# Kernel tuning notes

Measured on AMD Instinct MI355X. Metric: run time of the kernel, lower is better.

The kernel has to match this reference:

```python
import jax, jax.numpy as jnp
import numpy as np

NUM_TABLES = 26
NUM_ROWS = 50000
WIDTH = 128
BATCH = 4096
NNZ = 20
NUM_NUM = 13
MLP_SIZES = [512, 256, 128]


def setup_inputs() -> dict:
    key = jax.random.key(0)
    ks = jax.random.split(key, 16)
    numerical = jax.random.normal(ks[0], (BATCH, NUM_NUM), dtype=jnp.float32)
    cat = jax.random.randint(ks[1], (NUM_TABLES, BATCH, NNZ), 0, NUM_ROWS)
    tables = jax.random.normal(ks[2], (NUM_TABLES, NUM_ROWS, WIDTH), dtype=jnp.float32) * 0.01
    d_in = NUM_TABLES * WIDTH + NUM_NUM  # concat of pooled embeddings + numericals
    dims = [d_in] + MLP_SIZES + [1]
    inp = {"numerical": numerical, "cat": cat, "tables": tables}
    for i in range(len(dims) - 1):
        scale = 1.0 / np.sqrt(dims[i])
        inp[f"W{i+1}"] = jax.random.normal(ks[3 + i], (dims[i], dims[i + 1]), dtype=jnp.float32) * scale
        inp[f"b{i+1}"] = jnp.zeros((dims[i + 1],), dtype=jnp.float32)
    return inp


def reference(numerical, cat, tables, W1, b1, W2, b2, W3, b3, W4, b4):
    # Multi-table gather + reduce_sum: tables [T,R,W], cat [T,B,NNZ] -> pooled [T,B,W]
    pooled = jax.vmap(lambda T, idx: jnp.take(T, idx, axis=0).sum(axis=1))(tables, cat)
    # concat pooled tables (in input order) then numericals: [B, T*W + NUM_NUM]
    flat = pooled.transpose(1, 0, 2).reshape(pooled.shape[1], -1)
    x = jnp.concatenate([flat, numerical], axis=1)
    x = jax.nn.relu(x @ W1 + b1)
    x = jax.nn.relu(x @ W2 + b2)
    x = jax.nn.relu(x @ W3 + b3)
    return x @ W4 + b4  # [B, 1]
```

## Files before the change

kernel.cpp:

```cpp
#include <hip/hip_runtime.h>
#include <hip/hip_bf16.h>

#define T_NUM_TABLES 26
#define T_NUM_ROWS 50000
#define T_WIDTH 128
#define T_BATCH 4096
#define T_NNZ 20
#define T_NUM_NUM 13
#define T_DE (T_NUM_TABLES * T_WIDTH)

typedef __attribute__((ext_vector_type(4))) float f32x4;
typedef __attribute__((ext_vector_type(8))) short bf16x8;

#define PJ_POOL (512 * T_NUM_TABLES)
#define PJ_WT (PJ_POOL + 1664 + 128 + 32)
#define PJ_TOTAL (PJ_WT + T_BATCH)

__global__ void poolprep_v7(const float* __restrict__ tables,
                            const int* __restrict__ cat,
                            const float* __restrict__ W1, const float* __restrict__ W2,
                            const float* __restrict__ W3, const float* __restrict__ b1,
                            const float* __restrict__ b4, const float* __restrict__ num,
                            __hip_bfloat16* __restrict__ xh,
                            __hip_bfloat16* __restrict__ w1t, __hip_bfloat16* __restrict__ w2t,
                            __hip_bfloat16* __restrict__ w3t, float* __restrict__ c0,
                            float* __restrict__ out) {
  __shared__ int sidx[8][T_NNZ];
  __shared__ float tile[32][33];
  __shared__ float snum[T_NUM_NUM];
  const int bid = blockIdx.x;

  if (bid < PJ_POOL) {
    const int g = bid & 511;
    const int t = bid >> 9;
    const int b0 = g * 8;
    const int tx = threadIdx.x & 31;
    const int ty = threadIdx.x >> 5;
    if (threadIdx.x < 8 * T_NNZ) {
      int y = threadIdx.x / T_NNZ, j = threadIdx.x % T_NNZ;
      sidx[y][j] = cat[((size_t)t * T_BATCH + b0 + y) * T_NNZ + j];
    }
    __syncthreads();
    const f32x4* tb = (const f32x4*)(tables + (size_t)t * T_NUM_ROWS * T_WIDTH);
    f32x4 acc = {0.f, 0.f, 0.f, 0.f};
#pragma unroll
    for (int j = 0; j < T_NNZ; ++j) acc += tb[(size_t)sidx[ty][j] * 32 + tx];
    ushort4 u;
    {
      __hip_bfloat16 h0 = __float2bfloat16(acc[0]), h1 = __float2bfloat16(acc[1]);
      __hip_bfloat16 h2 = __float2bfloat16(acc[2]), h3 = __float2bfloat16(acc[3]);
      u.x = *(unsigned short*)&h0; u.y = *(unsigned short*)&h1;
      u.z = *(unsigned short*)&h2; u.w = *(unsigned short*)&h3;
    }
    *(ushort4*)(&xh[(size_t)(b0 + ty) * T_DE + t * T_WIDTH + tx * 4]) = u;
    return;
  }

  if (bid < PJ_WT) {
    int r = bid - PJ_POOL;
    const float* in;
    __hip_bfloat16* outt;
    int Kc, N, xb, yb;
    if (r < 1664)      { in = W1; outt = w1t; Kc = 3328; N = 512; xb = r % 104; yb = r / 104; }
    else if (r < 1792) { r -= 1664; in = W2; outt = w2t; Kc = 512; N = 256; xb = r % 16; yb = r / 16; }
    else               { r -= 1792; in = W3; outt = w3t; Kc = 256; N = 128; xb = r % 8;  yb = r / 8;  }
    int tx = threadIdx.x & 31, ty = threadIdx.x >> 5;
    int kb = xb * 32, nb = yb * 32;
    for (int rr = ty; rr < 32; rr += 8) tile[rr][tx] = in[(size_t)(kb + rr) * N + nb + tx];
    __syncthreads();
    for (int rr = ty; rr < 32; rr += 8)
      outt[(size_t)(nb + rr) * Kc + kb + tx] = __float2bfloat16(tile[tx][rr]);
    return;
  }

  {
    int b = bid - PJ_WT;
    if (threadIdx.x < T_NUM_NUM) snum[threadIdx.x] = num[b * T_NUM_NUM + threadIdx.x];
    if (threadIdx.x == 0) out[b] = b4[0];
    __syncthreads();
#pragma unroll
    for (int rep = 0; rep < 2; ++rep) {
      int n = threadIdx.x + rep * 256;
      float acc = b1[n];
#pragma unroll
      for (int j = 0; j < T_NUM_NUM; ++j)
        acc += snum[j] * W1[(size_t)(T_DE + j) * 512 + n];
      c0[(size_t)b * 512 + n] = acc;
    }
  }
}

template <int BM, int BN, int RELU, int MODE>
__global__ __launch_bounds__(256, 2) void gemm_v7(
    const __hip_bfloat16* __restrict__ A,
    const __hip_bfloat16* __restrict__ Bt,
    const float* __restrict__ bias1,
    const float* __restrict__ bias2d,
    const float* __restrict__ W4,
    __hip_bfloat16* __restrict__ Ch,
    float* __restrict__ outv,
    int M, int N, int Kp) {
  constexpr int MR = BM / 32, NR = BN / 32;
  constexpr int BUFB = BM * 128 + BN * 128;
  __shared__ char smem[2 * BUFB];

  const int tid = threadIdx.x;
  const int wave = tid >> 6;
  const int lane = tid & 63;
  const int m0 = blockIdx.x * BM;
  const int n0 = blockIdx.y * BN;
  const int wr = wave >> 1;
  const int wc = wave & 1;

  f32x4 acc[MR][NR] = {};
  const size_t strideA = (size_t)Kp * 2;

  auto stage = [&](int k0, int buf) {
    char* As = smem + buf * BUFB;
    char* Bs = As + BM * 128;
#pragma unroll
    for (int it = 0; it < BM / 32; ++it) {
      int chunk = wave + it * 4;
      int p = chunk * 1024 + lane * 16;
      int row = p >> 7, colb = p & 127;
      int colb_g = colb ^ ((row & 7) << 4);
      size_t goff = (size_t)(m0 + row) * strideA + (size_t)k0 * 2 + colb_g;
      __builtin_amdgcn_global_load_lds(
          (const __attribute__((address_space(1))) void*)((const char*)A + goff),
          (__attribute__((address_space(3))) void*)(As + chunk * 1024), 16, 0, 0);
    }
#pragma unroll
    for (int it = 0; it < BN / 32; ++it) {
      int chunk = wave + it * 4;
      int p = chunk * 1024 + lane * 16;
      int row = p >> 7, colb = p & 127;
      int colb_g = colb ^ ((row & 7) << 4);
      size_t goff = (size_t)(n0 + row) * strideA + (size_t)k0 * 2 + colb_g;
      __builtin_amdgcn_global_load_lds(
          (const __attribute__((address_space(1))) void*)((const char*)Bt + goff),
          (__attribute__((address_space(3))) void*)(Bs + chunk * 1024), 16, 0, 0);
    }
  };

  const int nt = Kp >> 6;
  stage(0, 0);
  __syncthreads();
  int cur = 0;
  for (int t = 0; t < nt; ++t) {
    if (t + 1 < nt) stage((t + 1) << 6, cur ^ 1);
    char* As = smem + cur * BUFB;
    char* Bs = As + BM * 128;
#pragma unroll
    for (int ks = 0; ks < 2; ++ks) {
      bf16x8 af[MR], bfr[NR];
      const int cb = (ks * 32 + ((lane >> 4) * 8)) * 2;
#pragma unroll
      for (int m = 0; m < MR; ++m) {
        int row = wr * (BM / 2) + m * 16 + (lane & 15);
        int addr = row * 128 + (cb ^ ((row & 7) << 4));
        af[m] = *(const bf16x8*)(As + addr);
      }
#pragma unroll
      for (int n = 0; n < NR; ++n) {
        int row = wc * (BN / 2) + n * 16 + (lane & 15);
        int addr = row * 128 + (cb ^ ((row & 7) << 4));
        bfr[n] = *(const bf16x8*)(Bs + addr);
      }
#pragma unroll
      for (int m = 0; m < MR; ++m)
#pragma unroll
        for (int n = 0; n < NR; ++n)
          acc[m][n] = __builtin_amdgcn_mfma_f32_16x16x32_bf16(af[m], bfr[n], acc[m][n], 0, 0, 0);
    }
    __syncthreads();
    cur ^= 1;
  }

#pragma unroll
  for (int m = 0; m < MR; ++m) {
#pragma unroll
    for (int n = 0; n < NR; ++n) {
      int col = n0 + wc * (BN / 2) + n * 16 + (lane & 15);
      float bv = bias1 ? bias1[col] : 0.f;
      float w4c = (MODE == 2) ? W4[col] : 0.f;
      float dot[4];
#pragma unroll
      for (int i = 0; i < 4; ++i) {
        int row = m0 + wr * (BM / 2) + m * 16 + ((lane >> 4) * 4) + i;
        float v = acc[m][n][i] + bv;
        if (bias2d) v += bias2d[(size_t)row * N + col];
        if (RELU) v = fmaxf(v, 0.f);
        if (MODE == 0) {
          Ch[(size_t)row * N + col] = __float2bfloat16(v);
        } else {
          dot[i] = v * w4c;
        }
      }
      if (MODE == 2) {
#pragma unroll
        for (int i = 0; i < 4; ++i) {
#pragma unroll
          for (int mask = 1; mask < 16; mask <<= 1) dot[i] += __shfl_xor(dot[i], mask);
        }
        if ((lane & 15) == 0) {
          int rowb = m0 + wr * (BM / 2) + m * 16 + ((lane >> 4) * 4);
#pragma unroll
          for (int i = 0; i < 4; ++i) atomicAdd(&outv[rowb + i], dot[i]);
        }
      }
    }
  }
}

extern "C" void kernel_launch(void* const* d_in, const int* in_sizes, int n_in,
                              void* d_out, int out_size, void* d_ws, size_t ws_size,
                              hipStream_t stream) {
  const float* numerical = (const float*)d_in[0];
  const int* cat = (const int*)d_in[1];
  const float* tables = (const float*)d_in[2];
  const float* W1 = (const float*)d_in[3];
  const float* b1 = (const float*)d_in[4];
  const float* W2 = (const float*)d_in[5];
  const float* b2 = (const float*)d_in[6];
  const float* W3 = (const float*)d_in[7];
  const float* b3 = (const float*)d_in[8];
  const float* W4 = (const float*)d_in[9];
  const float* b4 = (const float*)d_in[10];
  float* out = (float*)d_out;

  char* ws = (char*)d_ws;
  size_t off = 0;
  auto walloc = [&](size_t bytes) -> void* {
    void* p = ws + off;
    off = (off + bytes + 255) & ~(size_t)255;
    return p;
  };
  __hip_bfloat16* xh  = (__hip_bfloat16*)walloc((size_t)T_BATCH * T_DE * 2);
  __hip_bfloat16* w1t = (__hip_bfloat16*)walloc((size_t)512 * T_DE * 2);
  float*          c0  = (float*)walloc((size_t)T_BATCH * 512 * 4);
  __hip_bfloat16* a1  = (__hip_bfloat16*)walloc((size_t)T_BATCH * 512 * 2);
  __hip_bfloat16* w2t = (__hip_bfloat16*)walloc((size_t)256 * 512 * 2);
  __hip_bfloat16* a2  = (__hip_bfloat16*)walloc((size_t)T_BATCH * 256 * 2);
  __hip_bfloat16* w3t = (__hip_bfloat16*)walloc((size_t)128 * 256 * 2);

  poolprep_v7<<<PJ_TOTAL, 256, 0, stream>>>(tables, cat, W1, W2, W3, b1, b4, numerical,
                                            xh, w1t, w2t, w3t, c0, out);

  gemm_v7<64, 128, 1, 0><<<dim3(T_BATCH / 64, 512 / 128), 256, 0, stream>>>(
      xh, w1t, nullptr, c0, nullptr, a1, nullptr, T_BATCH, 512, T_DE);
  gemm_v7<64, 64, 1, 0><<<dim3(T_BATCH / 64, 256 / 64), 256, 0, stream>>>(
      a1, w2t, b2, nullptr, nullptr, a2, nullptr, T_BATCH, 256, 512);
  gemm_v7<64, 32, 1, 2><<<dim3(T_BATCH / 64, 128 / 32), 256, 0, stream>>>(
      a2, w3t, b3, nullptr, W4, nullptr, out, T_BATCH, 128, 256);
}
```

Baseline: 213.7 us.

## Prefetch two K-tiles ahead with explicit vmcnt waits and raise MFMA priority

The GEMM main loop now issues the next tile's async global-to-LDS loads before the loop. It waits with a counted s_waitcnt vmcnt so the following tile's loads stay in flight while the current tile is computed. After each tile it issues the load for the tile two steps ahead into the freed buffer, replacing the old synchronous double buffering. s_setprio is raised around the MFMA block to favour matrix issue, and the first GEMM's tile shrinks from 64x128 to 64x64, doubling its grid. The risks are higher reload traffic on the A operand and reliance on the vmcnt count matching the number of loads issued per stage.

After: 195.4 us. -8.6%, faster.

```diff
diff --git a/kernel.cpp b/kernel.cpp
--- a/kernel.cpp
+++ b/kernel.cpp
@@ -16,7 +16,7 @@
 #define PJ_WT (PJ_POOL + 1664 + 128 + 32)
 #define PJ_TOTAL (PJ_WT + T_BATCH)
 
-__global__ void poolprep_v7(const float* __restrict__ tables,
+__global__ void poolprep_v8(const float* __restrict__ tables,
                             const int* __restrict__ cat,
                             const float* __restrict__ W1, const float* __restrict__ W2,
                             const float* __restrict__ W3, const float* __restrict__ b1,
@@ -91,7 +91,7 @@
 }
 
 template <int BM, int BN, int RELU, int MODE>
-__global__ __launch_bounds__(256, 2) void gemm_v7(
+__global__ __launch_bounds__(256, 2) void gemm_v8(
     const __hip_bfloat16* __restrict__ A,
     const __hip_bfloat16* __restrict__ Bt,
     const float* __restrict__ bias1,
@@ -102,6 +102,7 @@
     int M, int N, int Kp) {
   constexpr int MR = BM / 32, NR = BN / 32;
   constexpr int BUFB = BM * 128 + BN * 128;
+  constexpr int L = BM / 32 + BN / 32;
   __shared__ char smem[2 * BUFB];
 
   const int tid = threadIdx.x;
@@ -144,10 +145,18 @@
 
   const int nt = Kp >> 6;
   stage(0, 0);
-  __syncthreads();
+  if (nt > 1) stage(64, 1);
   int cur = 0;
   for (int t = 0; t < nt; ++t) {
-    if (t + 1 < nt) stage((t + 1) << 6, cur ^ 1);
+    if (t + 1 < nt) {
+      asm volatile("s_waitcnt vmcnt(%0)" ::"n"(L) : "memory");
+    } else {
+      asm volatile("s_waitcnt vmcnt(0)" ::: "memory");
+    }
+    __builtin_amdgcn_sched_barrier(0);
+    __builtin_amdgcn_s_barrier();
+    __builtin_amdgcn_sched_barrier(0);
+
     char* As = smem + cur * BUFB;
     char* Bs = As + BM * 128;
 #pragma unroll
@@ -166,13 +175,19 @@
         int addr = row * 128 + (cb ^ ((row & 7) << 4));
         bfr[n] = *(const bf16x8*)(Bs + addr);
       }
+      __builtin_amdgcn_s_setprio(1);
 #pragma unroll
       for (int m = 0; m < MR; ++m)
 #pragma unroll
         for (int n = 0; n < NR; ++n)
           acc[m][n] = __builtin_amdgcn_mfma_f32_16x16x32_bf16(af[m], bfr[n], acc[m][n], 0, 0, 0);
-    }
-    __syncthreads();
+      __builtin_amdgcn_s_setprio(0);
+    }
+
+    __builtin_amdgcn_sched_barrier(0);
+    __builtin_amdgcn_s_barrier();
+    __builtin_amdgcn_sched_barrier(0);
+    if (t + 2 < nt) stage((t + 2) << 6, cur);
     cur ^= 1;
   }
 
@@ -243,13 +258,13 @@
   __hip_bfloat16* a2  = (__hip_bfloat16*)walloc((size_t)T_BATCH * 256 * 2);
   __hip_bfloat16* w3t = (__hip_bfloat16*)walloc((size_t)128 * 256 * 2);
 
-  poolprep_v7<<<PJ_TOTAL, 256, 0, stream>>>(tables, cat, W1, W2, W3, b1, b4, numerical,
+  poolprep_v8<<<PJ_TOTAL, 256, 0, stream>>>(tables, cat, W1, W2, W3, b1, b4, numerical,
                                             xh, w1t, w2t, w3t, c0, out);
 
-  gemm_v7<64, 128, 1, 0><<<dim3(T_BATCH / 64, 512 / 128), 256, 0, stream>>>(
+  gemm_v8<64, 64, 1, 0><<<dim3(T_BATCH / 64, 512 / 64), 256, 0, stream>>>(
       xh, w1t, nullptr, c0, nullptr, a1, nullptr, T_BATCH, 512, T_DE);
-  gemm_v7<64, 64, 1, 0><<<dim3(T_BATCH / 64, 256 / 64), 256, 0, stream>>>(
+  gemm_v8<64, 64, 1, 0><<<dim3(T_BATCH / 64, 256 / 64), 256, 0, stream>>>(
       a1, w2t, b2, nullptr, nullptr, a2, nullptr, T_BATCH, 256, 512);
-  gemm_v7<64, 32, 1, 2><<<dim3(T_BATCH / 64, 128 / 32), 256, 0, stream>>>(
+  gemm_v8<64, 32, 1, 2><<<dim3(T_BATCH / 64, 128 / 32), 256, 0, stream>>>(
       a2, w3t, b3, nullptr, W4, nullptr, out, T_BATCH, 128, 256);
 }
```
